# Kernel optimization log

Measured on AMD Instinct MI355X. Metric: run time of the kernel, lower is better.

The kernel has to match this reference:

```python
import jax, jax.numpy as jnp
import numpy as np

B, N, D = 4, 2048, 512

def setup_inputs() -> dict:
    key = jax.random.key(0)
    ks = jax.random.split(key, 7)
    s = 1.0 / np.sqrt(D)
    return {
        "x": jax.random.normal(ks[0], (B, N, D), dtype=jnp.float32),
        "Wq": jax.random.uniform(ks[1], (D, D), jnp.float32, -s, s),
        "bq": jax.random.uniform(ks[2], (D,), jnp.float32, -s, s),
        "Wk": jax.random.uniform(ks[3], (D, D), jnp.float32, -s, s),
        "bk": jax.random.uniform(ks[4], (D,), jnp.float32, -s, s),
        "Wv": jax.random.uniform(ks[5], (D, D), jnp.float32, -s, s),
        "bv": jax.random.uniform(ks[6], (D,), jnp.float32, -s, s),
    }

def reference(x, Wq, bq, Wk, bk, Wv, bv):
    # QKV projections (torch Linear: y = x @ W^T + b)
    q = jnp.einsum('bnd,ed->bne', x, Wq) + bq
    k = jnp.einsum('bnd,ed->bne', x, Wk) + bk
    v = jnp.einsum('bnd,ed->bne', x, Wv) + bv
    scale = 1.0 / jnp.sqrt(jnp.asarray(q.shape[-1], q.dtype))
    scores = jnp.einsum('bqd,bkd->bqk', q, k) * scale  # [B,N,N]
    weights = jax.nn.softmax(scores, axis=-1)
    return jnp.einsum('bqk,bkd->bqd', weights, v)
```

## Files before the change

kernel.cpp:

```cpp
#include <hip/hip_runtime.h>
#include <cstdint>
#include <cstddef>

#define SEQ 2048
#define DIM 512

using floatx4 = __attribute__((ext_vector_type(4))) float;
using halfx8  = __attribute__((ext_vector_type(8))) _Float16;

__device__ __forceinline__ ushort f2h(float f) {
    _Float16 h = (_Float16)f;
    return __builtin_bit_cast(unsigned short, h);
}

__global__ void prep_k(const float* __restrict__ x,
                       const float* __restrict__ Wq, const float* __restrict__ Wk,
                       const float* __restrict__ Wv,
                       const float* __restrict__ bq, const float* __restrict__ bk,
                       const float* __restrict__ bv,
                       ushort* __restrict__ xh, ushort* __restrict__ wcat,
                       float* __restrict__ bcat, float* __restrict__ rowsum) {
    int i = blockIdx.x * 256 + threadIdx.x;
    if (i < 1048576) {
        float4 v = ((const float4*)x)[i];
        ((ushort4*)xh)[i] = make_ushort4(f2h(v.x), f2h(v.y), f2h(v.z), f2h(v.w));
    } else if (i < 1048576 + 196608) {
        int j = i - 1048576;
        int which = j >> 16;
        const float* w = (which == 0) ? Wq : (which == 1) ? Wk : Wv;
        float4 v = ((const float4*)w)[j & 0xFFFF];
        ((ushort4*)wcat)[j] = make_ushort4(f2h(v.x), f2h(v.y), f2h(v.z), f2h(v.w));
    } else if (i < 1048576 + 196608 + 384) {
        int j = i - 1245184;
        const float* bsrc = (j < 128) ? bq : (j < 256) ? bk : bv;
        ((float4*)bcat)[j] = ((const float4*)bsrc)[j & 127];
    } else if (i < 1048576 + 196608 + 384 + 2048) {
        int j = i - 1245568;
        ((float4*)rowsum)[j] = (float4){0.f, 0.f, 0.f, 0.f};
    }
}


template<int EPI>
__global__ __launch_bounds__(256, 4)
void gemm_k(const ushort* __restrict__ A, const ushort* __restrict__ B,
            void* __restrict__ Cout, const float* __restrict__ bias,
            float* __restrict__ rowsum, ushort* __restrict__ vt,
            int lda, int ldb, int ldc, int kIters, float alpha,
            long sA, long sB, long sC)
{
    __shared__ __align__(16) ushort smem[2][2][4096];
    __shared__ float rsum[128];
    ushort* Ps = &smem[0][0][0];

    const int tid = threadIdx.x;
    const int bz = blockIdx.z;
    int b, kofs;
    if (EPI == 2) { b = bz & 3; kofs = (bz >> 2) * 512; }
    else          { b = bz; kofs = 0; }
    const ushort* Ab = A + (size_t)b * sA + kofs;
    const ushort* Bb = B + (size_t)b * sB + kofs;

    const int m0 = blockIdx.y * 128;
    const int n0 = blockIdx.x * 128;
    const int lane = tid & 63, wave = tid >> 6;
    const int wm = (wave >> 1) * 64, wn = (wave & 1) * 64;
    const int quad = lane >> 4, l16 = lane & 15;
    const int swz = (l16 >> 1) & 3;

    const int s0 = tid, s1 = tid + 256;
    const int r0 = s0 >> 2, r1 = s1 >> 2;
    const int kc0 = (s0 & 3) ^ ((r0 >> 1) & 3);
    const int kc1 = (s1 & 3) ^ ((r1 >> 1) & 3);
    const ushort* gA0 = Ab + (size_t)(m0 + r0) * lda + kc0 * 8;
    const ushort* gA1 = Ab + (size_t)(m0 + r1) * lda + kc1 * 8;
    const ushort* gB0 = Bb + (size_t)(n0 + r0) * ldb + kc0 * 8;
    const ushort* gB1 = Bb + (size_t)(n0 + r1) * ldb + kc1 * 8;

#define STAGE(kk, bufi) do {                                                              \
    int ko = (kk) * 32;                                                                   \
    __builtin_amdgcn_global_load_lds((const __attribute__((address_space(1))) uint32_t*)(gA0 + ko), \
        (__attribute__((address_space(3))) uint32_t*)(&smem[0][bufi][s0 * 8]), 16, 0, 0); \
    __builtin_amdgcn_global_load_lds((const __attribute__((address_space(1))) uint32_t*)(gA1 + ko), \
        (__attribute__((address_space(3))) uint32_t*)(&smem[0][bufi][s1 * 8]), 16, 0, 0); \
    __builtin_amdgcn_global_load_lds((const __attribute__((address_space(1))) uint32_t*)(gB0 + ko), \
        (__attribute__((address_space(3))) uint32_t*)(&smem[1][bufi][s0 * 8]), 16, 0, 0); \
    __builtin_amdgcn_global_load_lds((const __attribute__((address_space(1))) uint32_t*)(gB1 + ko), \
        (__attribute__((address_space(3))) uint32_t*)(&smem[1][bufi][s1 * 8]), 16, 0, 0); \
} while (0)

    int ofsA[4], ofsB[4];
#pragma unroll
    for (int mi = 0; mi < 4; mi++)
        ofsA[mi] = ((wm + mi * 16 + l16) * 4 + (quad ^ swz)) * 8;
#pragma unroll
    for (int ni = 0; ni < 4; ni++)
        ofsB[ni] = ((wn + ni * 16 + l16) * 4 + (quad ^ swz)) * 8;

    floatx4 acc[4][4];
#pragma unroll
    for (int i = 0; i < 4; i++)
#pragma unroll
        for (int j = 0; j < 4; j++)
            acc[i][j] = (floatx4){0.f, 0.f, 0.f, 0.f};

    if (EPI == 1 && tid < 128) rsum[tid] = 0.f;

    STAGE(0, 0);
    for (int it = 0; it < kIters; ++it) {
        __syncthreads();
        const int buf = it & 1;
        if (it + 1 < kIters) STAGE(it + 1, buf ^ 1);
        halfx8 af[4], bfr[4];
#pragma unroll
        for (int mi = 0; mi < 4; mi++) af[mi] = *(const halfx8*)&smem[0][buf][ofsA[mi]];
#pragma unroll
        for (int ni = 0; ni < 4; ni++) bfr[ni] = *(const halfx8*)&smem[1][buf][ofsB[ni]];
#pragma unroll
        for (int mi = 0; mi < 4; mi++)
#pragma unroll
            for (int ni = 0; ni < 4; ni++)
                acc[mi][ni] = __builtin_amdgcn_mfma_f32_16x16x32_f16(af[mi], bfr[ni], acc[mi][ni], 0, 0, 0);
    }
#undef STAGE

    if (EPI == 0 && n0 >= 1024) {
#pragma unroll
        for (int ni = 0; ni < 4; ni++) {
            int col = n0 + wn + ni * 16 + l16;
            float bv = bias[col];
            int e = col - 1024;
#pragma unroll
            for (int mi = 0; mi < 4; mi++) {
                int row0 = m0 + wm + mi * 16 + quad * 4;
                int bb = row0 >> 11;
                int j = row0 & 2047;
                ushort4 pk = make_ushort4(f2h(acc[mi][ni][0] + bv), f2h(acc[mi][ni][1] + bv),
                                          f2h(acc[mi][ni][2] + bv), f2h(acc[mi][ni][3] + bv));
                *(ushort4*)&vt[((size_t)(bb << 9) + e) * 2048 + j] = pk;
            }
        }
    } else {
        float bvv[4];
        if (EPI == 0) {
#pragma unroll
            for (int ni = 0; ni < 4; ni++) bvv[ni] = bias[n0 + wn + ni * 16 + l16];
        }
        float inv[4][4];
        if (EPI == 2) {
#pragma unroll
            for (int mi = 0; mi < 4; mi++)
#pragma unroll
                for (int r = 0; r < 4; r++)
                    inv[mi][r] = __builtin_amdgcn_rcpf(
                        rowsum[b * SEQ + m0 + wm + mi * 16 + quad * 4 + r]);
        }
        __syncthreads();
#pragma unroll
        for (int mi = 0; mi < 4; mi++)
#pragma unroll
            for (int ni = 0; ni < 4; ni++) {
                int col_l = wn + ni * 16 + l16;
                int c = col_l >> 3, w = col_l & 7;
#pragma unroll
                for (int r = 0; r < 4; r++) {
                    int row_l = wm + mi * 16 + quad * 4 + r;
                    float v = (EPI == 1) ? __expf(acc[mi][ni][r] * alpha)
                            : (EPI == 2) ? acc[mi][ni][r] * inv[mi][r]
                                         : acc[mi][ni][r] + bvv[ni];
                    Ps[row_l * 128 + ((c ^ (row_l & 7)) << 3) + w] = f2h(v);
                }
            }
        __syncthreads();
        int rr = tid >> 1, h = tid & 1;
        float s = 0.f;
        size_t base = (EPI == 1) ? (size_t)b * sC : (EPI == 2) ? (size_t)bz * sC : 0;
        ushort* dstrow = (ushort*)Cout + base + (size_t)(m0 + rr) * ldc + n0;
#pragma unroll
        for (int j = 0; j < 8; j++) {
            int c = h * 8 + j;
            halfx8 p = *(const halfx8*)&Ps[rr * 128 + ((c ^ (rr & 7)) << 3)];
            if (EPI == 1) {
#pragma unroll
                for (int e = 0; e < 8; e++) s += (float)p[e];
            }
            *(halfx8*)(dstrow + c * 8) = p;
        }
        if (EPI == 1) {
            atomicAdd(&rsum[rr], s);
            __syncthreads();
            if (tid < 128) atomicAdd(&rowsum[b * SEQ + m0 + tid], rsum[tid]);
        }
    }
}

__global__ void reduce_k(const ushort* __restrict__ part, float* __restrict__ out) {
    int t = blockIdx.x * 256 + threadIdx.x;
    size_t E = (size_t)t * 8;
    int b = (int)(E >> 20);
    size_t le = E & ((1u << 20) - 1);
    float acc[8] = {0,0,0,0,0,0,0,0};
#pragma unroll
    for (int kc = 0; kc < 4; kc++) {
        halfx8 p = *(const halfx8*)&part[(((size_t)(kc * 4 + b)) << 20) + le];
#pragma unroll
        for (int e = 0; e < 8; e++) acc[e] += (float)p[e];
    }
    float4 o0 = {acc[0], acc[1], acc[2], acc[3]};
    float4 o1 = {acc[4], acc[5], acc[6], acc[7]};
    ((float4*)(out + E))[0] = o0;
    ((float4*)(out + E))[1] = o1;
}

extern "C" void kernel_launch(void* const* d_in, const int* in_sizes, int n_in,
                              void* d_out, int out_size, void* d_ws, size_t ws_size,
                              hipStream_t stream) {
    const float* x  = (const float*)d_in[0];
    const float* Wq = (const float*)d_in[1];
    const float* bq = (const float*)d_in[2];
    const float* Wk = (const float*)d_in[3];
    const float* bk = (const float*)d_in[4];
    const float* Wv = (const float*)d_in[5];
    const float* bv = (const float*)d_in[6];
    float* out = (float*)d_out;
    char* ws = (char*)d_ws;

    ushort* partial = (ushort*)(ws);
    ushort* xh      = (ushort*)(ws);
    ushort* wcat    = (ushort*)(ws + 8388608);
    float*  bcat    = (float*)(ws + 9961472);
    float*  rowsum  = (float*)(ws + 33554432);
    ushort* Pb      = (ushort*)(ws + 33587200);
    ushort* vt      = (ushort*)(ws + 67141632);
    ushort* qkh     = (ushort*)(ws + 75530240);

    prep_k<<<4874, 256, 0, stream>>>(x, Wq, Wk, Wv, bq, bk, bv, xh, wcat, bcat, rowsum);

    gemm_k<0><<<dim3(12, 64, 1), 256, 0, stream>>>(
        xh, wcat, qkh, bcat, nullptr, vt, 512, 512, 1024, 16, 1.0f, 0, 0, 0);

    const float scale = 0.04419417382415922f;
    gemm_k<1><<<dim3(16, 16, 4), 256, 0, stream>>>(
        qkh, qkh + 512, Pb, nullptr, rowsum, nullptr, 1024, 1024, 2048, 16, scale,
        (long)SEQ * 1024, (long)SEQ * 1024, (long)SEQ * SEQ);

    gemm_k<2><<<dim3(4, 16, 16), 256, 0, stream>>>(
        Pb, vt, partial, nullptr, rowsum, nullptr, 2048, 2048, 512, 16, 1.0f,
        (long)SEQ * SEQ, (long)DIM * SEQ, (long)SEQ * DIM);

    reduce_k<<<2048, 256, 0, stream>>>(partial, out);
}
```

Measured before the change: 185.9 us.

## Enlarge GEMM block tile to 256x128 with 512 threads and two-pass epilogue

Doubles the M dimension of each GEMM block tile to 256 rows using 8 waves (512 threads), so each B tile loaded into LDS is reused by twice as many rows. The grids are halved in the M direction to match. The epilogue now stages the output through LDS in two 128-row passes. The EPI==1 row-sum reduction switches from LDS atomics to warp shuffles plus global atomics. The risks are fewer blocks in flight (halved grids) and larger per-block LDS and register pressure under launch_bounds(512,4).

```diff
diff --git a/kernel.cpp b/kernel.cpp
--- a/kernel.cpp
+++ b/kernel.cpp
@@ -42,16 +42,16 @@
 
 
 template<int EPI>
-__global__ __launch_bounds__(256, 4)
+__global__ __launch_bounds__(512, 4)
 void gemm_k(const ushort* __restrict__ A, const ushort* __restrict__ B,
             void* __restrict__ Cout, const float* __restrict__ bias,
             float* __restrict__ rowsum, ushort* __restrict__ vt,
             int lda, int ldb, int ldc, int kIters, float alpha,
             long sA, long sB, long sC)
 {
-    __shared__ __align__(16) ushort smem[2][2][4096];
-    __shared__ float rsum[128];
-    ushort* Ps = &smem[0][0][0];
+    __shared__ __align__(16) ushort As[2][8192];
+    __shared__ __align__(16) ushort Bs[2][4096];
+    ushort* Ps = &As[0][0];
 
     const int tid = threadIdx.x;
     const int bz = blockIdx.z;
@@ -61,32 +61,30 @@
     const ushort* Ab = A + (size_t)b * sA + kofs;
     const ushort* Bb = B + (size_t)b * sB + kofs;
 
-    const int m0 = blockIdx.y * 128;
+    const int m0 = blockIdx.y * 256;
     const int n0 = blockIdx.x * 128;
     const int lane = tid & 63, wave = tid >> 6;
     const int wm = (wave >> 1) * 64, wn = (wave & 1) * 64;
     const int quad = lane >> 4, l16 = lane & 15;
     const int swz = (l16 >> 1) & 3;
 
-    const int s0 = tid, s1 = tid + 256;
-    const int r0 = s0 >> 2, r1 = s1 >> 2;
-    const int kc0 = (s0 & 3) ^ ((r0 >> 1) & 3);
-    const int kc1 = (s1 & 3) ^ ((r1 >> 1) & 3);
-    const ushort* gA0 = Ab + (size_t)(m0 + r0) * lda + kc0 * 8;
-    const ushort* gA1 = Ab + (size_t)(m0 + r1) * lda + kc1 * 8;
-    const ushort* gB0 = Bb + (size_t)(n0 + r0) * ldb + kc0 * 8;
-    const ushort* gB1 = Bb + (size_t)(n0 + r1) * ldb + kc1 * 8;
+    const int sA0 = tid, sA1 = tid + 512, sBs = tid;
+    const int rA0 = sA0 >> 2, rA1 = sA1 >> 2, rB = sBs >> 2;
+    const int kA0 = (sA0 & 3) ^ ((rA0 >> 1) & 3);
+    const int kA1 = (sA1 & 3) ^ ((rA1 >> 1) & 3);
+    const int kB  = (sBs & 3) ^ ((rB  >> 1) & 3);
+    const ushort* gA0 = Ab + (size_t)(m0 + rA0) * lda + kA0 * 8;
+    const ushort* gA1 = Ab + (size_t)(m0 + rA1) * lda + kA1 * 8;
+    const ushort* gB0 = Bb + (size_t)(n0 + rB) * ldb + kB * 8;
 
 #define STAGE(kk, bufi) do {                                                              \
     int ko = (kk) * 32;                                                                   \
     __builtin_amdgcn_global_load_lds((const __attribute__((address_space(1))) uint32_t*)(gA0 + ko), \
-        (__attribute__((address_space(3))) uint32_t*)(&smem[0][bufi][s0 * 8]), 16, 0, 0); \
+        (__attribute__((address_space(3))) uint32_t*)(&As[bufi][sA0 * 8]), 16, 0, 0);     \
     __builtin_amdgcn_global_load_lds((const __attribute__((address_space(1))) uint32_t*)(gA1 + ko), \
-        (__attribute__((address_space(3))) uint32_t*)(&smem[0][bufi][s1 * 8]), 16, 0, 0); \
+        (__attribute__((address_space(3))) uint32_t*)(&As[bufi][sA1 * 8]), 16, 0, 0);     \
     __builtin_amdgcn_global_load_lds((const __attribute__((address_space(1))) uint32_t*)(gB0 + ko), \
-        (__attribute__((address_space(3))) uint32_t*)(&smem[1][bufi][s0 * 8]), 16, 0, 0); \
-    __builtin_amdgcn_global_load_lds((const __attribute__((address_space(1))) uint32_t*)(gB1 + ko), \
-        (__attribute__((address_space(3))) uint32_t*)(&smem[1][bufi][s1 * 8]), 16, 0, 0); \
+        (__attribute__((address_space(3))) uint32_t*)(&Bs[bufi][sBs * 8]), 16, 0, 0);     \
 } while (0)
 
     int ofsA[4], ofsB[4];
@@ -103,8 +101,6 @@
 #pragma unroll
         for (int j = 0; j < 4; j++)
             acc[i][j] = (floatx4){0.f, 0.f, 0.f, 0.f};
-
-    if (EPI == 1 && tid < 128) rsum[tid] = 0.f;
 
     STAGE(0, 0);
     for (int it = 0; it < kIters; ++it) {
@@ -113,9 +109,9 @@
         if (it + 1 < kIters) STAGE(it + 1, buf ^ 1);
         halfx8 af[4], bfr[4];
 #pragma unroll
-        for (int mi = 0; mi < 4; mi++) af[mi] = *(const halfx8*)&smem[0][buf][ofsA[mi]];
-#pragma unroll
-        for (int ni = 0; ni < 4; ni++) bfr[ni] = *(const halfx8*)&smem[1][buf][ofsB[ni]];
+        for (int mi = 0; mi < 4; mi++) af[mi] = *(const halfx8*)&As[buf][ofsA[mi]];
+#pragma unroll
+        for (int ni = 0; ni < 4; ni++) bfr[ni] = *(const halfx8*)&Bs[buf][ofsB[ni]];
 #pragma unroll
         for (int mi = 0; mi < 4; mi++)
 #pragma unroll
@@ -155,41 +151,48 @@
                     inv[mi][r] = __builtin_amdgcn_rcpf(
                         rowsum[b * SEQ + m0 + wm + mi * 16 + quad * 4 + r]);
         }
+        size_t base = (EPI == 1) ? (size_t)b * sC : (EPI == 2) ? (size_t)bz * sC : 0;
         __syncthreads();
 #pragma unroll
-        for (int mi = 0; mi < 4; mi++)
-#pragma unroll
-            for (int ni = 0; ni < 4; ni++) {
-                int col_l = wn + ni * 16 + l16;
-                int c = col_l >> 3, w = col_l & 7;
-#pragma unroll
-                for (int r = 0; r < 4; r++) {
-                    int row_l = wm + mi * 16 + quad * 4 + r;
-                    float v = (EPI == 1) ? __expf(acc[mi][ni][r] * alpha)
-                            : (EPI == 2) ? acc[mi][ni][r] * inv[mi][r]
-                                         : acc[mi][ni][r] + bvv[ni];
-                    Ps[row_l * 128 + ((c ^ (row_l & 7)) << 3) + w] = f2h(v);
+        for (int p = 0; p < 2; ++p) {
+            if ((wm >> 7) == p) {
+                int wml = wm & 127;
+#pragma unroll
+                for (int mi = 0; mi < 4; mi++)
+#pragma unroll
+                    for (int ni = 0; ni < 4; ni++) {
+                        int col_l = wn + ni * 16 + l16;
+                        int c = col_l >> 3, w = col_l & 7;
+#pragma unroll
+                        for (int r = 0; r < 4; r++) {
+                            int row_l = wml + mi * 16 + quad * 4 + r;
+                            float v = (EPI == 1) ? __expf(acc[mi][ni][r] * alpha)
+                                    : (EPI == 2) ? acc[mi][ni][r] * inv[mi][r]
+                                                 : acc[mi][ni][r] + bvv[ni];
+                            Ps[row_l * 128 + ((c ^ (row_l & 7)) << 3) + w] = f2h(v);
+                        }
+                    }
+            }
+            __syncthreads();
+            int rr = tid >> 2, t3 = tid & 3;
+            float s = 0.f;
+            ushort* dstrow = (ushort*)Cout + base + (size_t)(m0 + p * 128 + rr) * ldc + n0;
+#pragma unroll
+            for (int j = 0; j < 4; j++) {
+                int c = j * 4 + t3;
+                halfx8 pv = *(const halfx8*)&Ps[rr * 128 + ((c ^ (rr & 7)) << 3)];
+                if (EPI == 1) {
+#pragma unroll
+                    for (int e = 0; e < 8; e++) s += (float)pv[e];
                 }
-            }
-        __syncthreads();
-        int rr = tid >> 1, h = tid & 1;
-        float s = 0.f;
-        size_t base = (EPI == 1) ? (size_t)b * sC : (EPI == 2) ? (size_t)bz * sC : 0;
-        ushort* dstrow = (ushort*)Cout + base + (size_t)(m0 + rr) * ldc + n0;
-#pragma unroll
-        for (int j = 0; j < 8; j++) {
-            int c = h * 8 + j;
-            halfx8 p = *(const halfx8*)&Ps[rr * 128 + ((c ^ (rr & 7)) << 3)];
+                *(halfx8*)(dstrow + c * 8) = pv;
+            }
             if (EPI == 1) {
-#pragma unroll
-                for (int e = 0; e < 8; e++) s += (float)p[e];
-            }
-            *(halfx8*)(dstrow + c * 8) = p;
-        }
-        if (EPI == 1) {
-            atomicAdd(&rsum[rr], s);
+                s += __shfl_xor(s, 1);
+                s += __shfl_xor(s, 2);
+                if (t3 == 0) atomicAdd(&rowsum[b * SEQ + m0 + p * 128 + rr], s);
+            }
             __syncthreads();
-            if (tid < 128) atomicAdd(&rowsum[b * SEQ + m0 + tid], rsum[tid]);
         }
     }
 }
@@ -236,15 +239,15 @@
 
     prep_k<<<4874, 256, 0, stream>>>(x, Wq, Wk, Wv, bq, bk, bv, xh, wcat, bcat, rowsum);
 
-    gemm_k<0><<<dim3(12, 64, 1), 256, 0, stream>>>(
+    gemm_k<0><<<dim3(12, 32, 1), 512, 0, stream>>>(
         xh, wcat, qkh, bcat, nullptr, vt, 512, 512, 1024, 16, 1.0f, 0, 0, 0);
 
     const float scale = 0.04419417382415922f;
-    gemm_k<1><<<dim3(16, 16, 4), 256, 0, stream>>>(
+    gemm_k<1><<<dim3(16, 8, 4), 512, 0, stream>>>(
         qkh, qkh + 512, Pb, nullptr, rowsum, nullptr, 1024, 1024, 2048, 16, scale,
         (long)SEQ * 1024, (long)SEQ * 1024, (long)SEQ * SEQ);
 
-    gemm_k<2><<<dim3(4, 16, 16), 256, 0, stream>>>(
+    gemm_k<2><<<dim3(4, 8, 16), 512, 0, stream>>>(
         Pb, vt, partial, nullptr, rowsum, nullptr, 2048, 2048, 512, 16, 1.0f,
         (long)SEQ * SEQ, (long)DIM * SEQ, (long)SEQ * DIM);
 
```

After: 178.2 us. 1.04x faster.
